# Kernel tuning notes

Hardware: AMD Instinct MI355X
Metric: run time of the kernel (lower is better)

## Reference

```python
import jax, jax.numpy as jnp
import numpy as np

B, S, D, E, K = 4, 4096, 2048, 16, 2
TEMPERATURE = 1.0


def setup_inputs() -> dict:
    key = jax.random.key(0)
    ks = jax.random.split(key, 4)
    scale = 1.0 / np.sqrt(D)
    return {
        "x": jax.random.normal(ks[0], (B, S, D), dtype=jnp.float32),
        "w_route": jax.random.normal(ks[1], (D, E), dtype=jnp.float32) * scale,
        "b_route": jnp.zeros((E,), dtype=jnp.float32),
        "w_noise": jax.random.normal(ks[2], (D, E), dtype=jnp.float32) * scale,
        "b_noise": jnp.zeros((E,), dtype=jnp.float32),
        "eps": jax.random.normal(ks[3], (B, S, E), dtype=jnp.float32),
    }


def reference(x, w_route, b_route, w_noise, b_noise, eps):
    # dual linear projections: (B,S,D) @ (D,E) -> (B,S,E)
    logits = jnp.einsum("bsd,de->bse", x, w_route) + b_route
    noise_logits = jnp.einsum("bsd,de->bse", x, w_noise) + b_noise
    noise_scale = jax.nn.softplus(noise_logits)
    scaled_logits = (logits + eps * noise_scale) / TEMPERATURE

    top_k_logits, indices = jax.lax.top_k(scaled_logits, K)  # (B,S,K)
    # scatter top-k back over -inf, equivalent to masking non-topk entries
    in_topk = jax.nn.one_hot(indices, E, dtype=jnp.bool_).any(axis=-2)  # (B,S,E)
    sparse_logits = jnp.where(in_topk, scaled_logits, -jnp.inf)
    router_output = jax.nn.softmax(sparse_logits, axis=-1)

    router_prob = router_output.mean(axis=(0, 1))
    target = 1.0 / E
    aux_loss = jnp.sum((router_prob - target) ** 2)
    return router_output, indices, aux_loss
```

## Files before the change

### kernel.cpp

```cpp
#include <hip/hip_runtime.h>
#include <math.h>


#define DDIM 2048
#define NEXP 16
#define IDX_OFF 262144
#define AUX_OFF 294912

#define FMA_ROW(WPA, GG, i) { \
    const float4 xv = *(const float4*)(xb + (rg + 8 * (i)) * 16 + (((GG) ^ sw) << 2)); \
    acc[i].x = fmaf(xv.w, WPA[3].x, fmaf(xv.z, WPA[2].x, fmaf(xv.y, WPA[1].x, fmaf(xv.x, WPA[0].x, acc[i].x)))); \
    acc[i].y = fmaf(xv.w, WPA[3].y, fmaf(xv.z, WPA[2].y, fmaf(xv.y, WPA[1].y, fmaf(xv.x, WPA[0].y, acc[i].y)))); \
    acc[i].z = fmaf(xv.w, WPA[3].z, fmaf(xv.z, WPA[2].z, fmaf(xv.y, WPA[1].z, fmaf(xv.x, WPA[0].z, acc[i].z)))); \
    acc[i].w = fmaf(xv.w, WPA[3].w, fmaf(xv.z, WPA[2].w, fmaf(xv.y, WPA[1].w, fmaf(xv.x, WPA[0].w, acc[i].w)))); }

template<int NS>
__global__ __launch_bounds__(256) void gemv_k(
    const float* __restrict__ x, const float* __restrict__ wr,
    const float* __restrict__ wn, float* __restrict__ pbase) {
  constexpr int WAVE_DS = 512 / NS;
  constexpr int NCHNK = WAVE_DS / 16;
  __shared__ float smem[9216];

  const int tid  = threadIdx.x;
  const int wave = tid >> 6;
  const int lane = tid & 63;
  const int rg   = lane >> 3;
  const int q    = lane & 7;
  const int sw   = rg >> 1;
  const int rowtile = blockIdx.x / NS;
  const int dslice  = blockIdx.x % NS;
  const int row_base = rowtile * 64;
  const int d_base   = dslice * (DDIM / NS) + wave * WAVE_DS;

  float* xregion = smem + wave * 2048;

  const int srow  = lane >> 2;
  const int squad = lane & 3;
  const float* xsrc = x + (size_t)(row_base + srow) * DDIM + d_base + squad * 4;
  const int lwoff = srow * 16 + ((squad ^ ((srow >> 1) & 3)) << 2);

  const float* wbase = (q < 4 ? wr : wn) + (size_t)d_base * NEXP + (q & 3) * 4;

  float4 acc[8];
  #pragma unroll
  for (int i = 0; i < 8; ++i) acc[i] = make_float4(0.f, 0.f, 0.f, 0.f);

  float4 wp0[4], wp1[4];
  float4 xp[4];

  #pragma unroll
  for (int j = 0; j < 4; ++j) wp0[j] = *(const float4*)(wbase + j * NEXP);
  #pragma unroll
  for (int j = 0; j < 4; ++j) wp1[j] = *(const float4*)(wbase + 64 + j * NEXP);
  #pragma unroll
  for (int t = 0; t < 4; ++t) xp[t] = *(const float4*)(xsrc + (size_t)t * 16 * DDIM);
  #pragma unroll
  for (int t = 0; t < 4; ++t) *(float4*)(xregion + lwoff + t * 256) = xp[t];

  for (int k = 0; k < NCHNK; ++k) {
    const float* xb = xregion + (k & 1) * 1024;
    if (k + 1 < NCHNK) {
      #pragma unroll
      for (int t = 0; t < 4; ++t)
        xp[t] = *(const float4*)(xsrc + (size_t)t * 16 * DDIM + (k + 1) * 16);
    }
    #pragma unroll
    for (int i = 0; i < 8; ++i) FMA_ROW(wp0, 0, i);
    { const float* wl = wbase + (size_t)(4 * k + 2) * 64;
      #pragma unroll
      for (int j = 0; j < 4; ++j) wp0[j] = *(const float4*)(wl + j * NEXP); }
    #pragma unroll
    for (int i = 0; i < 8; ++i) FMA_ROW(wp1, 1, i);
    { const float* wl = wbase + (size_t)(4 * k + 3) * 64;
      #pragma unroll
      for (int j = 0; j < 4; ++j) wp1[j] = *(const float4*)(wl + j * NEXP); }
    #pragma unroll
    for (int i = 0; i < 8; ++i) FMA_ROW(wp0, 2, i);
    if (k + 1 < NCHNK) {
      const float* wl = wbase + (size_t)(4 * k + 4) * 64;
      #pragma unroll
      for (int j = 0; j < 4; ++j) wp0[j] = *(const float4*)(wl + j * NEXP);
    }
    #pragma unroll
    for (int i = 0; i < 8; ++i) FMA_ROW(wp1, 3, i);
    if (k + 1 < NCHNK) {
      const float* wl = wbase + (size_t)(4 * k + 5) * 64;
      #pragma unroll
      for (int j = 0; j < 4; ++j) wp1[j] = *(const float4*)(wl + j * NEXP);
      float* xw = xregion + ((k + 1) & 1) * 1024;
      #pragma unroll
      for (int t = 0; t < 4; ++t) *(float4*)(xw + lwoff + t * 256) = xp[t];
    }
  }

  {
    float* pr = xregion;
    const int psw = (q ^ rg) << 2;
    #pragma unroll
    for (int i = 0; i < 8; ++i)
      *(float4*)(pr + (rg + 8 * i) * 32 + psw) = acc[i];
  }
  __syncthreads();

  float* pws = pbase + (size_t)(dslice * 256 + rowtile) * 2048;
  #pragma unroll
  for (int u = 0; u < 2; ++u) {
    const int f   = tid * 2 + u;
    const int row = f >> 3;
    const int g   = f & 7;
    const int off = row * 32 + ((g ^ (row & 7)) << 2);
    float4 a0 = *(const float4*)(smem + 0 * 2048 + off);
    float4 a1 = *(const float4*)(smem + 1 * 2048 + off);
    float4 a2 = *(const float4*)(smem + 2 * 2048 + off);
    float4 a3 = *(const float4*)(smem + 3 * 2048 + off);
    float4 s = make_float4((a0.x + a1.x) + (a2.x + a3.x),
                           (a0.y + a1.y) + (a2.y + a3.y),
                           (a0.z + a1.z) + (a2.z + a3.z),
                           (a0.w + a1.w) + (a2.w + a3.w));
    *(float4*)(pws + row * 32 + g * 4) = s;
  }
}

template<int NS>
__global__ __launch_bounds__(64) void epi_k(
    const float* __restrict__ pbase, const float* __restrict__ br,
    const float* __restrict__ bn, const float* __restrict__ eps,
    float* __restrict__ out, float* __restrict__ auxs) {
  const int lane = threadIdx.x;
  const int bid  = blockIdx.x;
  const int row_g = bid * 64 + lane;

  float c[32];
  #pragma unroll
  for (int g = 0; g < 8; ++g) {
    float4 a = make_float4(0.f, 0.f, 0.f, 0.f);
    #pragma unroll
    for (int s = 0; s < NS; ++s) {
      float4 p = *(const float4*)(pbase + (size_t)(s * 256 + bid) * 2048 + lane * 32 + g * 4);
      a.x += p.x; a.y += p.y; a.z += p.z; a.w += p.w;
    }
    c[g * 4 + 0] = a.x; c[g * 4 + 1] = a.y; c[g * 4 + 2] = a.z; c[g * 4 + 3] = a.w;
  }

  float brv[16], bnv[16], ev[16];
  #pragma unroll
  for (int g = 0; g < 4; ++g) {
    *(float4*)(brv + g * 4) = *(const float4*)(br + g * 4);
    *(float4*)(bnv + g * 4) = *(const float4*)(bn + g * 4);
    *(float4*)(ev  + g * 4) = *(const float4*)(eps + (size_t)row_g * NEXP + g * 4);
  }

  float s[16];
  #pragma unroll
  for (int e = 0; e < 16; ++e) {
    float lg = c[e] + brv[e];
    float nz = c[16 + e] + bnv[e];
    float sp = fmaxf(nz, 0.f) + log1pf(expf(-fabsf(nz)));
    s[e] = lg + ev[e] * sp;
  }

  float b1 = s[0]; int i1 = 0;
  #pragma unroll
  for (int e = 1; e < 16; ++e) { if (s[e] > b1) { b1 = s[e]; i1 = e; } }
  float b2 = -INFINITY; int i2 = 0;
  #pragma unroll
  for (int e = 0; e < 16; ++e) { if (e != i1 && s[e] > b2) { b2 = s[e]; i2 = e; } }

  float t2 = expf(b2 - b1);
  float p1 = 1.f / (1.f + t2);
  float p2 = t2 / (1.f + t2);

  float v[16];
  #pragma unroll
  for (int e = 0; e < 16; ++e)
    v[e] = (e == i1) ? p1 : ((e == i2) ? p2 : 0.f);

  float* orow = out + (size_t)row_g * NEXP;
  *(float4*)(orow + 0)  = make_float4(v[0], v[1], v[2], v[3]);
  *(float4*)(orow + 4)  = make_float4(v[4], v[5], v[6], v[7]);
  *(float4*)(orow + 8)  = make_float4(v[8], v[9], v[10], v[11]);
  *(float4*)(orow + 12) = make_float4(v[12], v[13], v[14], v[15]);

  float* oidx = out + IDX_OFF + (size_t)row_g * 2;
  *(float2*)oidx = make_float2((float)i1, (float)i2);

  #pragma unroll
  for (int m = 1; m < 64; m <<= 1) {
    #pragma unroll
    for (int e = 0; e < 16; ++e) v[e] += __shfl_xor(v[e], m, 64);
  }
  if (lane == 0) {
    float* ap = auxs + (size_t)bid * 16;
    *(float4*)(ap + 0)  = make_float4(v[0], v[1], v[2], v[3]);
    *(float4*)(ap + 4)  = make_float4(v[4], v[5], v[6], v[7]);
    *(float4*)(ap + 8)  = make_float4(v[8], v[9], v[10], v[11]);
    *(float4*)(ap + 12) = make_float4(v[12], v[13], v[14], v[15]);
  }
}

__global__ void router_aux_k(const float* __restrict__ auxs, float* __restrict__ out_aux) {
  __shared__ float red[16][17];
  __shared__ float sq[16];
  const int t = threadIdx.x;
  const int e = t & 15;
  const int g = t >> 4;
  float ssum = 0.f;
  #pragma unroll
  for (int b = 0; b < 16; ++b) ssum += auxs[(size_t)(g * 16 + b) * 16 + e];
  red[g][e] = ssum;
  __syncthreads();
  if (t < 16) {
    float tot = 0.f;
    #pragma unroll
    for (int gg = 0; gg < 16; ++gg) tot += red[gg][t];
    float diff = tot * (1.f / 16384.f) - 0.0625f;
    sq[t] = diff * diff;
  }
  __syncthreads();
  if (t == 0) {
    float a = 0.f;
    #pragma unroll
    for (int i = 0; i < 16; ++i) a += sq[i];
    *out_aux = a;
  }
}

extern "C" void kernel_launch(void* const* d_in, const int* in_sizes, int n_in,
                              void* d_out, int out_size, void* d_ws, size_t ws_size,
                              hipStream_t stream) {
  const float* x   = (const float*)d_in[0];
  const float* wr  = (const float*)d_in[1];
  const float* br  = (const float*)d_in[2];
  const float* wn  = (const float*)d_in[3];
  const float* bn  = (const float*)d_in[4];
  const float* eps = (const float*)d_in[5];
  float* out = (float*)d_out;

  float* wsf   = (float*)d_ws;
  float* auxs  = wsf;
  float* pbase = wsf + 4096;

  const size_t need4 = (size_t)(4096 + 4 * 524288) * 4;
  const size_t need2 = (size_t)(4096 + 2 * 524288) * 4;

  if (ws_size >= need4) {
    gemv_k<4><<<1024, 256, 0, stream>>>(x, wr, wn, pbase);
    epi_k<4><<<256, 64, 0, stream>>>(pbase, br, bn, eps, out, auxs);
  } else if (ws_size >= need2) {
    gemv_k<2><<<512, 256, 0, stream>>>(x, wr, wn, pbase);
    epi_k<2><<<256, 64, 0, stream>>>(pbase, br, bn, eps, out, auxs);
  } else {
    gemv_k<1><<<256, 256, 0, stream>>>(x, wr, wn, pbase);
    epi_k<1><<<256, 64, 0, stream>>>(pbase, br, bn, eps, out, auxs);
  }
  router_aux_k<<<1, 256, 0, stream>>>(auxs, out + AUX_OFF);
}
```

Before: 60.68 us.

## Replace FP32 FMA GEMV with split-bf16 MFMA emulation of FP32 projection

The scalar FMA routing projection is replaced by a matrix-core kernel. Each FP32 operand is split into three bf16 parts (high, mid, low), and six cross-term MFMA 16x16x32 bf16 products per operand pair approximate FP32 accuracy. A new pre-kernel converts both weight matrices each call into transposed split-bf16 planes in the workspace, and x is split in registers. This targets the FMA compute cost, at the price of an extra launch, extra MFMA work, and possible small precision differences that could flip top-k ties.

```diff
diff --git a/kernel.cpp b/kernel.cpp
--- a/kernel.cpp
+++ b/kernel.cpp
@@ -2,123 +2,113 @@
 #include <math.h>
 
 
-#define DDIM 2048
 #define NEXP 16
 #define IDX_OFF 262144
 #define AUX_OFF 294912
-
-#define FMA_ROW(WPA, GG, i) { \
-    const float4 xv = *(const float4*)(xb + (rg + 8 * (i)) * 16 + (((GG) ^ sw) << 2)); \
-    acc[i].x = fmaf(xv.w, WPA[3].x, fmaf(xv.z, WPA[2].x, fmaf(xv.y, WPA[1].x, fmaf(xv.x, WPA[0].x, acc[i].x)))); \
-    acc[i].y = fmaf(xv.w, WPA[3].y, fmaf(xv.z, WPA[2].y, fmaf(xv.y, WPA[1].y, fmaf(xv.x, WPA[0].y, acc[i].y)))); \
-    acc[i].z = fmaf(xv.w, WPA[3].z, fmaf(xv.z, WPA[2].z, fmaf(xv.y, WPA[1].z, fmaf(xv.x, WPA[0].z, acc[i].z)))); \
-    acc[i].w = fmaf(xv.w, WPA[3].w, fmaf(xv.z, WPA[2].w, fmaf(xv.y, WPA[1].w, fmaf(xv.x, WPA[0].w, acc[i].w)))); }
+#define WT_FLOATS 98304
+
+typedef __attribute__((ext_vector_type(8))) short short8v;
+typedef __attribute__((ext_vector_type(4))) float f32x4;
+
+__global__ __launch_bounds__(256) void conv_k(
+    const float* __restrict__ wr, const float* __restrict__ wn,
+    unsigned short* __restrict__ wt) {
+  const int e  = blockIdx.x >> 3;
+  const int k  = (blockIdx.x & 7) * 256 + threadIdx.x;
+  const float* src = (e < 16) ? (wr + e) : (wn + (e - 16));
+  float f = src[(size_t)k * 16];
+  unsigned u  = __float_as_uint(f);
+  unsigned hu = u & 0xffff0000u;
+  float r1 = f - __uint_as_float(hu);
+  unsigned mu = __float_as_uint(r1) & 0xffff0000u;
+  float r2 = r1 - __uint_as_float(mu);
+  unsigned lu = __float_as_uint(r2);
+  wt[0 * 65536 + e * 2048 + k] = (unsigned short)(hu >> 16);
+  wt[1 * 65536 + e * 2048 + k] = (unsigned short)(mu >> 16);
+  wt[2 * 65536 + e * 2048 + k] = (unsigned short)(lu >> 16);
+}
 
 template<int NS>
-__global__ __launch_bounds__(256) void gemv_k(
-    const float* __restrict__ x, const float* __restrict__ wr,
-    const float* __restrict__ wn, float* __restrict__ pbase) {
-  constexpr int WAVE_DS = 512 / NS;
-  constexpr int NCHNK = WAVE_DS / 16;
+__global__ __launch_bounds__(256) void gemm_k(
+    const float* __restrict__ x, const unsigned short* __restrict__ wt,
+    float* __restrict__ pbase) {
+  constexpr int KS = 2048 / NS;
+  constexpr int NSTEP = KS / 32;
   __shared__ float smem[9216];
 
   const int tid  = threadIdx.x;
   const int wave = tid >> 6;
   const int lane = tid & 63;
-  const int rg   = lane >> 3;
-  const int q    = lane & 7;
-  const int sw   = rg >> 1;
-  const int rowtile = blockIdx.x / NS;
-  const int dslice  = blockIdx.x % NS;
-  const int row_base = rowtile * 64;
-  const int d_base   = dslice * (DDIM / NS) + wave * WAVE_DS;
-
-  float* xregion = smem + wave * 2048;
-
-  const int srow  = lane >> 2;
-  const int squad = lane & 3;
-  const float* xsrc = x + (size_t)(row_base + srow) * DDIM + d_base + squad * 4;
-  const int lwoff = srow * 16 + ((squad ^ ((srow >> 1) & 3)) << 2);
-
-  const float* wbase = (q < 4 ? wr : wn) + (size_t)d_base * NEXP + (q & 3) * 4;
-
-  float4 acc[8];
-  #pragma unroll
-  for (int i = 0; i < 8; ++i) acc[i] = make_float4(0.f, 0.f, 0.f, 0.f);
-
-  float4 wp0[4], wp1[4];
-  float4 xp[4];
-
-  #pragma unroll
-  for (int j = 0; j < 4; ++j) wp0[j] = *(const float4*)(wbase + j * NEXP);
-  #pragma unroll
-  for (int j = 0; j < 4; ++j) wp1[j] = *(const float4*)(wbase + 64 + j * NEXP);
-  #pragma unroll
-  for (int t = 0; t < 4; ++t) xp[t] = *(const float4*)(xsrc + (size_t)t * 16 * DDIM);
-  #pragma unroll
-  for (int t = 0; t < 4; ++t) *(float4*)(xregion + lwoff + t * 256) = xp[t];
-
-  for (int k = 0; k < NCHNK; ++k) {
-    const float* xb = xregion + (k & 1) * 1024;
-    if (k + 1 < NCHNK) {
-      #pragma unroll
-      for (int t = 0; t < 4; ++t)
-        xp[t] = *(const float4*)(xsrc + (size_t)t * 16 * DDIM + (k + 1) * 16);
+  const int l15  = lane & 15;
+  const int kg   = lane >> 4;
+  const int rowblk = blockIdx.x / NS;
+  const int slice  = blockIdx.x % NS;
+
+  const int row = rowblk * 64 + wave * 16 + l15;
+  const float* xp = x + (size_t)row * 2048 + slice * KS + kg * 8;
+
+  const size_t wl_off = (size_t)slice * KS + kg * 8;
+  const unsigned short* ph0 = wt + 0 * 65536 + (l15)      * 2048 + wl_off;
+  const unsigned short* ph1 = wt + 0 * 65536 + (16 + l15) * 2048 + wl_off;
+  const unsigned short* pm0 = wt + 1 * 65536 + (l15)      * 2048 + wl_off;
+  const unsigned short* pm1 = wt + 1 * 65536 + (16 + l15) * 2048 + wl_off;
+  const unsigned short* pl0 = wt + 2 * 65536 + (l15)      * 2048 + wl_off;
+  const unsigned short* pl1 = wt + 2 * 65536 + (16 + l15) * 2048 + wl_off;
+
+  f32x4 accR = {0.f, 0.f, 0.f, 0.f};
+  f32x4 accN = {0.f, 0.f, 0.f, 0.f};
+
+  for (int s = 0; s < NSTEP; ++s) {
+    float4 xa = *(const float4*)(xp + s * 32);
+    float4 xb = *(const float4*)(xp + s * 32 + 4);
+    short8v bh0 = *(const short8v*)(ph0 + (size_t)s * 32);
+    short8v bh1 = *(const short8v*)(ph1 + (size_t)s * 32);
+    short8v bm0 = *(const short8v*)(pm0 + (size_t)s * 32);
+    short8v bm1 = *(const short8v*)(pm1 + (size_t)s * 32);
+    short8v bl0 = *(const short8v*)(pl0 + (size_t)s * 32);
+    short8v bl1 = *(const short8v*)(pl1 + (size_t)s * 32);
+    short8v xh, xm, xl;
+    float f[8] = {xa.x, xa.y, xa.z, xa.w, xb.x, xb.y, xb.z, xb.w};
+    #pragma unroll
+    for (int j = 0; j < 8; ++j) {
+      unsigned u  = __float_as_uint(f[j]);
+      unsigned hu = u & 0xffff0000u;
+      float r1 = f[j] - __uint_as_float(hu);
+      unsigned mu = __float_as_uint(r1) & 0xffff0000u;
+      float r2 = r1 - __uint_as_float(mu);
+      unsigned lu = __float_as_uint(r2);
+      xh[j] = (short)(hu >> 16);
+      xm[j] = (short)(mu >> 16);
+      xl[j] = (short)(lu >> 16);
     }
-    #pragma unroll
-    for (int i = 0; i < 8; ++i) FMA_ROW(wp0, 0, i);
-    { const float* wl = wbase + (size_t)(4 * k + 2) * 64;
-      #pragma unroll
-      for (int j = 0; j < 4; ++j) wp0[j] = *(const float4*)(wl + j * NEXP); }
-    #pragma unroll
-    for (int i = 0; i < 8; ++i) FMA_ROW(wp1, 1, i);
-    { const float* wl = wbase + (size_t)(4 * k + 3) * 64;
-      #pragma unroll
-      for (int j = 0; j < 4; ++j) wp1[j] = *(const float4*)(wl + j * NEXP); }
-    #pragma unroll
-    for (int i = 0; i < 8; ++i) FMA_ROW(wp0, 2, i);
-    if (k + 1 < NCHNK) {
-      const float* wl = wbase + (size_t)(4 * k + 4) * 64;
-      #pragma unroll
-      for (int j = 0; j < 4; ++j) wp0[j] = *(const float4*)(wl + j * NEXP);
-    }
-    #pragma unroll
-    for (int i = 0; i < 8; ++i) FMA_ROW(wp1, 3, i);
-    if (k + 1 < NCHNK) {
-      const float* wl = wbase + (size_t)(4 * k + 5) * 64;
-      #pragma unroll
-      for (int j = 0; j < 4; ++j) wp1[j] = *(const float4*)(wl + j * NEXP);
-      float* xw = xregion + ((k + 1) & 1) * 1024;
-      #pragma unroll
-      for (int t = 0; t < 4; ++t) *(float4*)(xw + lwoff + t * 256) = xp[t];
-    }
-  }
-
-  {
-    float* pr = xregion;
-    const int psw = (q ^ rg) << 2;
-    #pragma unroll
-    for (int i = 0; i < 8; ++i)
-      *(float4*)(pr + (rg + 8 * i) * 32 + psw) = acc[i];
-  }
-  __syncthreads();
-
-  float* pws = pbase + (size_t)(dslice * 256 + rowtile) * 2048;
+    accR = __builtin_amdgcn_mfma_f32_16x16x32_bf16(xh, bh0, accR, 0, 0, 0);
+    accN = __builtin_amdgcn_mfma_f32_16x16x32_bf16(xh, bh1, accN, 0, 0, 0);
+    accR = __builtin_amdgcn_mfma_f32_16x16x32_bf16(xm, bh0, accR, 0, 0, 0);
+    accN = __builtin_amdgcn_mfma_f32_16x16x32_bf16(xm, bh1, accN, 0, 0, 0);
+    accR = __builtin_amdgcn_mfma_f32_16x16x32_bf16(xl, bh0, accR, 0, 0, 0);
+    accN = __builtin_amdgcn_mfma_f32_16x16x32_bf16(xl, bh1, accN, 0, 0, 0);
+    accR = __builtin_amdgcn_mfma_f32_16x16x32_bf16(xh, bm0, accR, 0, 0, 0);
+    accN = __builtin_amdgcn_mfma_f32_16x16x32_bf16(xh, bm1, accN, 0, 0, 0);
+    accR = __builtin_amdgcn_mfma_f32_16x16x32_bf16(xm, bm0, accR, 0, 0, 0);
+    accN = __builtin_amdgcn_mfma_f32_16x16x32_bf16(xm, bm1, accN, 0, 0, 0);
+    accR = __builtin_amdgcn_mfma_f32_16x16x32_bf16(xh, bl0, accR, 0, 0, 0);
+    accN = __builtin_amdgcn_mfma_f32_16x16x32_bf16(xh, bl1, accN, 0, 0, 0);
+  }
+
+  float* tile = smem + wave * 576;
+  #pragma unroll
+  for (int j = 0; j < 4; ++j) {
+    tile[(kg * 4 + j) * 36 + l15]      = accR[j];
+    tile[(kg * 4 + j) * 36 + 16 + l15] = accN[j];
+  }
+  float* po = pbase + (size_t)slice * 524288 + ((size_t)rowblk * 64 + wave * 16) * 32;
   #pragma unroll
   for (int u = 0; u < 2; ++u) {
-    const int f   = tid * 2 + u;
-    const int row = f >> 3;
-    const int g   = f & 7;
-    const int off = row * 32 + ((g ^ (row & 7)) << 2);
-    float4 a0 = *(const float4*)(smem + 0 * 2048 + off);
-    float4 a1 = *(const float4*)(smem + 1 * 2048 + off);
-    float4 a2 = *(const float4*)(smem + 2 * 2048 + off);
-    float4 a3 = *(const float4*)(smem + 3 * 2048 + off);
-    float4 s = make_float4((a0.x + a1.x) + (a2.x + a3.x),
-                           (a0.y + a1.y) + (a2.y + a3.y),
-                           (a0.z + a1.z) + (a2.z + a3.z),
-                           (a0.w + a1.w) + (a2.w + a3.w));
-    *(float4*)(pws + row * 32 + g * 4) = s;
+    const int idx = lane * 8 + u * 4;
+    const int r = idx >> 5;
+    const int c = idx & 31;
+    float4 v = *(const float4*)(tile + r * 36 + c);
+    *(float4*)(po + idx) = v;
   }
 }
 
@@ -137,7 +127,7 @@
     float4 a = make_float4(0.f, 0.f, 0.f, 0.f);
     #pragma unroll
     for (int s = 0; s < NS; ++s) {
-      float4 p = *(const float4*)(pbase + (size_t)(s * 256 + bid) * 2048 + lane * 32 + g * 4);
+      float4 p = *(const float4*)(pbase + (size_t)s * 524288 + (size_t)row_g * 32 + g * 4);
       a.x += p.x; a.y += p.y; a.z += p.z; a.w += p.w;
     }
     c[g * 4 + 0] = a.x; c[g * 4 + 1] = a.y; c[g * 4 + 2] = a.z; c[g * 4 + 3] = a.w;
@@ -237,21 +227,23 @@
   const float* eps = (const float*)d_in[5];
   float* out = (float*)d_out;
 
-  float* wsf   = (float*)d_ws;
-  float* auxs  = wsf;
-  float* pbase = wsf + 4096;
-
-  const size_t need4 = (size_t)(4096 + 4 * 524288) * 4;
-  const size_t need2 = (size_t)(4096 + 2 * 524288) * 4;
-
+  float* wsf = (float*)d_ws;
+  float* auxs = wsf;
+  unsigned short* wt = (unsigned short*)(wsf + 4096);
+  float* pbase = wsf + 4096 + WT_FLOATS;
+
+  const size_t need4 = (size_t)(4096 + WT_FLOATS + 4 * 524288) * 4;
+  const size_t need2 = (size_t)(4096 + WT_FLOATS + 2 * 524288) * 4;
+
+  conv_k<<<256, 256, 0, stream>>>(wr, wn, wt);
   if (ws_size >= need4) {
-    gemv_k<4><<<1024, 256, 0, stream>>>(x, wr, wn, pbase);
+    gemm_k<4><<<1024, 256, 0, stream>>>(x, wt, pbase);
     epi_k<4><<<256, 64, 0, stream>>>(pbase, br, bn, eps, out, auxs);
   } else if (ws_size >= need2) {
-    gemv_k<2><<<512, 256, 0, stream>>>(x, wr, wn, pbase);
+    gemm_k<2><<<512, 256, 0, stream>>>(x, wt, pbase);
     epi_k<2><<<256, 64, 0, stream>>>(pbase, br, bn, eps, out, auxs);
   } else {
-    gemv_k<1><<<256, 256, 0, stream>>>(x, wr, wn, pbase);
+    gemm_k<1><<<256, 256, 0, stream>>>(x, wt, pbase);
     epi_k<1><<<256, 64, 0, stream>>>(pbase, br, bn, eps, out, auxs);
   }
   router_aux_k<<<1, 256, 0, stream>>>(auxs, out + AUX_OFF);
```

After: 78.92 us. 1.3x slower.
